# Optimization experiments

Hardware: AMD Instinct MI355X
Metric: run time of the kernel (lower is better)

The kernel has to match this reference:

```python
import jax, jax.numpy as jnp
import numpy as np

D_MODEL = 1024
NHEAD = 16
D_K = D_MODEL // NHEAD


def setup_inputs() -> dict:
    key = jax.random.key(0)
    ks = jax.random.split(key, 11)
    B, S = 2, 2048
    scale = 1.0 / np.sqrt(D_MODEL)
    inp = {
        "q": jax.random.normal(ks[0], (B, S, D_MODEL), jnp.float32),
        "k": jax.random.normal(ks[1], (B, S, D_MODEL), jnp.float32),
        "v": jax.random.normal(ks[2], (B, S, D_MODEL), jnp.float32),
        "Wq": jax.random.normal(ks[3], (D_MODEL, D_MODEL), jnp.float32) * scale,
        "bq": jnp.zeros((D_MODEL,), jnp.float32),
        "Wk": jax.random.normal(ks[4], (D_MODEL, D_MODEL), jnp.float32) * scale,
        "bk": jnp.zeros((D_MODEL,), jnp.float32),
        "Wv": jax.random.normal(ks[5], (D_MODEL, D_MODEL), jnp.float32) * scale,
        "bv": jnp.zeros((D_MODEL,), jnp.float32),
        "Wo": jax.random.normal(ks[6], (D_MODEL, D_MODEL), jnp.float32) * scale,
        "bo": jnp.zeros((D_MODEL,), jnp.float32),
    }
    return inp


def reference(q, k, v, Wq, bq, Wk, bk, Wv, bv, Wo, bo):
    B, S, _ = q.shape
    # Linear projections (torch Linear: x @ W.T + b), split into heads
    def proj(x, W, b):
        y = jnp.einsum('bsd,ed->bse', x, W) + b
        return y.reshape(B, -1, NHEAD, D_K).transpose(0, 2, 1, 3)  # [B,H,S,Dk]

    qh = proj(q, Wq, bq)
    kh = proj(k, Wk, bk)
    vh = proj(v, Wv, bv)

    scores = jnp.einsum('bhqd,bhkd->bhqk', qh, kh) / jnp.sqrt(
        jnp.asarray(D_K, qh.dtype))
    attn = jax.nn.softmax(scores, axis=-1)  # dropout is identity in eval
    out = jnp.einsum('bhqk,bhkd->bhqd', attn, vh)
    out = out.transpose(0, 2, 1, 3).reshape(B, S, D_MODEL)
    return jnp.einsum('bsd,ed->bse', out, Wo) + bo
```

## Files before the change

### kernel.cpp

```cpp
#include <hip/hip_runtime.h>
#include <stdint.h>
#include <stddef.h>

#define D_MODEL 1024
#define NHEAD   16
#define DK      64
#define BB      2
#define SS      2048
#define NTOK    (BB*SS)

#define SCALE_Q 0.18033688011f

typedef short  short8 __attribute__((ext_vector_type(8)));
typedef __bf16 bf16x8 __attribute__((ext_vector_type(8)));
typedef float  f32x4  __attribute__((ext_vector_type(4)));

__device__ __forceinline__ unsigned short f2bf(float x){
  unsigned int u = __builtin_bit_cast(unsigned int, x);
  u += 0x7fffu + ((u >> 16) & 1u);
  return (unsigned short)(u >> 16);
}

__device__ __forceinline__ unsigned int pack_bf2(float x, float y){
  unsigned int a = __builtin_bit_cast(unsigned int, x) + 0x8000u;
  unsigned int b = __builtin_bit_cast(unsigned int, y) + 0x8000u;
  return __builtin_amdgcn_perm(b, a, 0x07060302u);
}

__device__ __forceinline__ float fast_exp2(float x){
#if __has_builtin(__builtin_amdgcn_exp2f)
  return __builtin_amdgcn_exp2f(x);
#else
  return exp2f(x);
#endif
}

__device__ __forceinline__ f32x4 mfma16(bf16x8 a, bf16x8 b, f32x4 c){
  return __builtin_amdgcn_mfma_f32_16x16x32_bf16(a, b, c, 0, 0, 0);
}

__device__ __forceinline__ void async16(const void* g, void* lds){
  __builtin_amdgcn_global_load_lds(
      (const __attribute__((address_space(1))) unsigned int*)g,
      (__attribute__((address_space(3))) unsigned int*)lds,
      16, 0, 0);
}

__global__ __launch_bounds__(256) void cast_bf16_all(
    const float* __restrict__ q,  const float* __restrict__ k,  const float* __restrict__ v,
    const float* __restrict__ wq, const float* __restrict__ wk, const float* __restrict__ wv,
    const float* __restrict__ wo,
    unsigned short* __restrict__ qb,  unsigned short* __restrict__ kb,  unsigned short* __restrict__ vb,
    unsigned short* __restrict__ wqb, unsigned short* __restrict__ wkb, unsigned short* __restrict__ wvb,
    unsigned short* __restrict__ wob)
{
  const float* src; unsigned short* dst; int n;
  switch (blockIdx.y){
    case 0: src = q;  dst = qb;  n = NTOK*D_MODEL;    break;
    case 1: src = k;  dst = kb;  n = NTOK*D_MODEL;    break;
    case 2: src = v;  dst = vb;  n = NTOK*D_MODEL;    break;
    case 3: src = wq; dst = wqb; n = D_MODEL*D_MODEL; break;
    case 4: src = wk; dst = wkb; n = D_MODEL*D_MODEL; break;
    case 5: src = wv; dst = wvb; n = D_MODEL*D_MODEL; break;
    default: src = wo; dst = wob; n = D_MODEL*D_MODEL; break;
  }
  int i = (blockIdx.x * 256 + threadIdx.x) * 8;
  if (i >= n) return;
  float4 a = *(const float4*)(src + i);
  float4 b = *(const float4*)(src + i + 4);
  short8 o;
  o[0] = (short)f2bf(a.x); o[1] = (short)f2bf(a.y);
  o[2] = (short)f2bf(a.z); o[3] = (short)f2bf(a.w);
  o[4] = (short)f2bf(b.x); o[5] = (short)f2bf(b.y);
  o[6] = (short)f2bf(b.z); o[7] = (short)f2bf(b.w);
  *(short8*)(dst + i) = o;
}

__global__ __launch_bounds__(256) void qkv_gemm(
    const unsigned short* __restrict__ qb, const unsigned short* __restrict__ kb,
    const unsigned short* __restrict__ vb,
    const unsigned short* __restrict__ wqb, const unsigned short* __restrict__ wkb,
    const unsigned short* __restrict__ wvb,
    const float* __restrict__ bq, const float* __restrict__ bk, const float* __restrict__ bv,
    unsigned short* __restrict__ Qh, unsigned short* __restrict__ Kh, unsigned short* __restrict__ Vt)
{
  __shared__ __align__(16) unsigned short As[128*32];
  __shared__ __align__(16) unsigned short Bs[128*32];
  const int id = blockIdx.x, z = id >> 8, r = id & 255;
  const unsigned short *A, *Bt; const float* bias; unsigned short* C;
  int bm, bn, N, brow; float scale;
  if (z == 0){ A = qb;  Bt = wqb; bias = bq; C = Qh; bm = (r>>3)*128; bn = (r&7)*128; N = 1024; brow = 0; scale = SCALE_Q; }
  else if (z == 1){ A = kb;  Bt = wkb; bias = bk; C = Kh; bm = (r>>3)*128; bn = (r&7)*128; N = 1024; brow = 0; scale = 1.0f; }
  else            { A = wvb; Bt = vb;  bias = bv; C = Vt; bm = (r&7)*128; bn = (r>>3)*128; N = 4096; brow = 1; scale = 1.0f; }
  const int K = 1024;
  const int tid  = threadIdx.x, lane = tid & 63, w = tid >> 6;
  const int quad = lane >> 4,   l16  = lane & 15;
  const int wm = w >> 1, wn = w & 1;
  const int sw = l16 & 3;
  f32x4 acc[4][4] = {};
  for (int kb_ = 0; kb_ < (K >> 5); ++kb_){
    const int k0 = kb_ << 5;
    __syncthreads();
    #pragma unroll
    for (int c = 0; c < 2; ++c){
      int chunk = (w*2 + c)*64 + lane;
      int row = chunk >> 2, c4 = chunk & 3;
      int cs = (c4 ^ (row & 3)) << 3;
      async16(A  + (size_t)(bm + row)*K + k0 + cs, (char*)As + (w*2 + c)*1024);
      async16(Bt + (size_t)(bn + row)*K + k0 + cs, (char*)Bs + (w*2 + c)*1024);
    }
    __syncthreads();
    bf16x8 af[4], bf[4];
    #pragma unroll
    for (int mt = 0; mt < 4; ++mt)
      af[mt] = *(const bf16x8*)&As[(wm*64 + mt*16 + l16)*32 + ((quad ^ sw) << 3)];
    #pragma unroll
    for (int nt = 0; nt < 4; ++nt)
      bf[nt] = *(const bf16x8*)&Bs[(wn*64 + nt*16 + l16)*32 + ((quad ^ sw) << 3)];
    #pragma unroll
    for (int mt = 0; mt < 4; ++mt)
      #pragma unroll
      for (int nt = 0; nt < 4; ++nt)
        acc[mt][nt] = mfma16(af[mt], bf[nt], acc[mt][nt]);
  }
  const int m0 = bm + wm*64, n0 = bn + wn*64;
  #pragma unroll
  for (int mt = 0; mt < 4; ++mt){
    #pragma unroll
    for (int nt = 0; nt < 4; ++nt){
      int col = n0 + nt*16 + l16;
      float bc = brow ? 0.0f : bias[col];
      #pragma unroll
      for (int rr = 0; rr < 4; ++rr){
        int row = m0 + mt*16 + quad*4 + rr;
        float val = (acc[mt][nt][rr] + (brow ? bias[row] : bc)) * scale;
        C[(size_t)row*N + col] = f2bf(val);
      }
    }
  }
}

__global__ __launch_bounds__(256) void gemm_out(
    const unsigned short* __restrict__ A, const unsigned short* __restrict__ Bt,
    const float* __restrict__ bias, float* __restrict__ C)
{
  __shared__ __align__(16) unsigned short As[64*32];
  __shared__ __align__(16) unsigned short Bs[128*32];
  const int K = 1024, N = 1024;
  const int tid  = threadIdx.x, lane = tid & 63, w = tid >> 6;
  const int quad = lane >> 4,   l16  = lane & 15;
  const int bm = blockIdx.y * 64, bn = blockIdx.x * 128;
  const int sw = l16 & 3;
  f32x4 acc[4][2] = {};
  for (int kb_ = 0; kb_ < (K >> 5); ++kb_){
    const int k0 = kb_ << 5;
    __syncthreads();
    {
      int chunk = w*64 + lane;
      int row = chunk >> 2, c4 = chunk & 3;
      async16(A + (size_t)(bm + row)*K + k0 + ((c4 ^ (row & 3)) << 3),
              (char*)As + w*1024);
    }
    #pragma unroll
    for (int c = 0; c < 2; ++c){
      int chunk = (w*2 + c)*64 + lane;
      int row = chunk >> 2, c4 = chunk & 3;
      async16(Bt + (size_t)(bn + row)*K + k0 + ((c4 ^ (row & 3)) << 3),
              (char*)Bs + (w*2 + c)*1024);
    }
    __syncthreads();
    bf16x8 af[4], bf[2];
    #pragma unroll
    for (int mt = 0; mt < 4; ++mt)
      af[mt] = *(const bf16x8*)&As[(mt*16 + l16)*32 + ((quad ^ sw) << 3)];
    #pragma unroll
    for (int nt = 0; nt < 2; ++nt)
      bf[nt] = *(const bf16x8*)&Bs[(w*32 + nt*16 + l16)*32 + ((quad ^ sw) << 3)];
    #pragma unroll
    for (int mt = 0; mt < 4; ++mt)
      #pragma unroll
      for (int nt = 0; nt < 2; ++nt)
        acc[mt][nt] = mfma16(af[mt], bf[nt], acc[mt][nt]);
  }
  #pragma unroll
  for (int mt = 0; mt < 4; ++mt){
    #pragma unroll
    for (int nt = 0; nt < 2; ++nt){
      int col = bn + w*32 + nt*16 + l16;
      float bc = bias[col];
      #pragma unroll
      for (int rr = 0; rr < 4; ++rr){
        int row = bm + mt*16 + quad*4 + rr;
        C[(size_t)row*N + col] = acc[mt][nt][rr] + bc;
      }
    }
  }
}

__global__ __launch_bounds__(256) void attn(
    const unsigned short* __restrict__ Qh, const unsigned short* __restrict__ Kh,
    const unsigned short* __restrict__ Vt, unsigned short* __restrict__ ctx)
{
  __shared__ __align__(16) unsigned short Kbuf[64*64];
  __shared__ __align__(16) unsigned short Vbuf[64*64];
  __shared__ __align__(16) unsigned short QP[128*64];

  const int tid  = threadIdx.x, lane = tid & 63, w = tid >> 6;
  const int quad = lane >> 4,   l16  = lane & 15;
  const int b = blockIdx.y >> 4, h = blockIdx.y & 15;
  const int q0 = blockIdx.x * 128;
  const int sw = l16 & 7;

  #pragma unroll
  for (int c = 0; c < 4; ++c){
    int s = (w*4 + c)*64 + lane;
    int row = s >> 3, c8 = s & 7;
    async16(Qh + (size_t)(b*SS + q0 + row)*D_MODEL + h*DK + ((c8 ^ (row & 7)) << 3),
            (char*)QP + (w*4 + c)*1024);
  }
  __syncthreads();
  bf16x8 bq[2][2];
  #pragma unroll
  for (int qg = 0; qg < 2; ++qg)
    #pragma unroll
    for (int ks = 0; ks < 2; ++ks)
      bq[qg][ks] = *(const bf16x8*)&QP[(w*32 + qg*16 + l16)*64 + (((ks*4 + quad) ^ sw) << 3)];

  const unsigned short* Kp = Kh + (size_t)(b*SS)*D_MODEL + h*DK;
  const unsigned short* Vp = Vt + (size_t)(h*DK)*NTOK + b*SS;
  const unsigned short* ksrc[2];
  const unsigned short* vsrc[2];
  #pragma unroll
  for (int c = 0; c < 2; ++c){
    int s = (w*2 + c)*64 + lane;
    int row = s >> 3, c8 = s & 7;
    int cs = (c8 ^ (row & 7)) << 3;
    ksrc[c] = Kp + (size_t)row*D_MODEL + cs;
    vsrc[c] = Vp + (size_t)row*NTOK  + cs;
  }

  f32x4 acc[2][4] = {};
  float l_i[2] = {0.0f, 0.0f};

  for (int kv0 = 0; kv0 < SS; kv0 += 64){
    __syncthreads();
    #pragma unroll
    for (int c = 0; c < 2; ++c){
      async16(ksrc[c], (char*)Kbuf + (w*2 + c)*1024);
      async16(vsrc[c], (char*)Vbuf + (w*2 + c)*1024);
      ksrc[c] += 64*D_MODEL;
      vsrc[c] += 64;
    }
    __syncthreads();

    bf16x8 kf[4][2];
    #pragma unroll
    for (int mt = 0; mt < 4; ++mt)
      #pragma unroll
      for (int ks = 0; ks < 2; ++ks)
        kf[mt][ks] = *(const bf16x8*)&Kbuf[(mt*16 + l16)*64 + (((ks*4 + quad) ^ sw) << 3)];
    f32x4 s0[4] = {}, s1[4] = {};
    #pragma unroll
    for (int mt = 0; mt < 4; ++mt)
      #pragma unroll
      for (int ks = 0; ks < 2; ++ks){
        s0[mt] = mfma16(kf[mt][ks], bq[0][ks], s0[mt]);
        s1[mt] = mfma16(kf[mt][ks], bq[1][ks], s1[mt]);
      }

    float ls0 = 0.0f, ls1 = 0.0f;
    #pragma unroll
    for (int mt = 0; mt < 4; ++mt)
      #pragma unroll
      for (int rr = 0; rr < 4; ++rr){
        float p0 = fast_exp2(s0[mt][rr]); s0[mt][rr] = p0; ls0 += p0;
        float p1 = fast_exp2(s1[mt][rr]); s1[mt][rr] = p1; ls1 += p1;
      }
    l_i[0] += ls0; l_i[1] += ls1;
    const int pr0 = (w*32 +      l16)*64;
    const int pr1 = (w*32 + 16 + l16)*64;
    #pragma unroll
    for (int mt = 0; mt < 4; ++mt){
      int c8  = mt*2 + (quad >> 1);
      int off = ((c8 ^ sw) << 3) + (quad & 1)*4;
      uint2 p;
      p.x = pack_bf2(s0[mt][0], s0[mt][1]);
      p.y = pack_bf2(s0[mt][2], s0[mt][3]);
      *(uint2*)&QP[pr0 + off] = p;
      p.x = pack_bf2(s1[mt][0], s1[mt][1]);
      p.y = pack_bf2(s1[mt][2], s1[mt][3]);
      *(uint2*)&QP[pr1 + off] = p;
    }
    asm volatile("s_waitcnt lgkmcnt(0)" ::: "memory");

    bf16x8 bp[2][2];
    #pragma unroll
    for (int qg = 0; qg < 2; ++qg)
      #pragma unroll
      for (int ks = 0; ks < 2; ++ks)
        bp[qg][ks] = *(const bf16x8*)&QP[(w*32 + qg*16 + l16)*64 + (((ks*4 + quad) ^ sw) << 3)];
    bf16x8 vf[4][2];
    #pragma unroll
    for (int nt = 0; nt < 4; ++nt)
      #pragma unroll
      for (int ks = 0; ks < 2; ++ks)
        vf[nt][ks] = *(const bf16x8*)&Vbuf[(nt*16 + l16)*64 + (((ks*4 + quad) ^ sw) << 3)];
    #pragma unroll
    for (int nt = 0; nt < 4; ++nt)
      #pragma unroll
      for (int ks = 0; ks < 2; ++ks){
        acc[0][nt] = mfma16(vf[nt][ks], bp[0][ks], acc[0][nt]);
        acc[1][nt] = mfma16(vf[nt][ks], bp[1][ks], acc[1][nt]);
      }
  }

  float inv[2];
  #pragma unroll
  for (int qg = 0; qg < 2; ++qg){
    float t = l_i[qg];
    t += __shfl_xor(t, 16);
    t += __shfl_xor(t, 32);
    inv[qg] = 1.0f / t;
  }
  #pragma unroll
  for (int qg = 0; qg < 2; ++qg){
    int pr = (w*32 + qg*16 + l16)*64;
    #pragma unroll
    for (int nt = 0; nt < 4; ++nt){
      int c8  = nt*2 + (quad >> 1);
      int off = ((c8 ^ sw) << 3) + (quad & 1)*4;
      uint2 p;
      p.x = pack_bf2(acc[qg][nt][0]*inv[qg], acc[qg][nt][1]*inv[qg]);
      p.y = pack_bf2(acc[qg][nt][2]*inv[qg], acc[qg][nt][3]*inv[qg]);
      *(uint2*)&QP[pr + off] = p;
    }
  }
  asm volatile("s_waitcnt lgkmcnt(0)" ::: "memory");
  {
    int r  = w*32 + (lane >> 1);
    int j0 = (lane & 1)*4;
    unsigned short* dst = ctx + (size_t)(b*SS + q0 + r)*D_MODEL + h*DK;
    #pragma unroll
    for (int i = 0; i < 4; ++i){
      int j = j0 + i;
      uint4 d = *(const uint4*)&QP[r*64 + ((j ^ (r & 7)) << 3)];
      *(uint4*)(dst + j*8) = d;
    }
  }
}

extern "C" void kernel_launch(void* const* d_in, const int* in_sizes, int n_in,
                              void* d_out, int out_size, void* d_ws, size_t ws_size,
                              hipStream_t stream) {
  const float* q  = (const float*)d_in[0];
  const float* k  = (const float*)d_in[1];
  const float* v  = (const float*)d_in[2];
  const float* Wq = (const float*)d_in[3];
  const float* bq = (const float*)d_in[4];
  const float* Wk = (const float*)d_in[5];
  const float* bk = (const float*)d_in[6];
  const float* Wv = (const float*)d_in[7];
  const float* bv = (const float*)d_in[8];
  const float* Wo = (const float*)d_in[9];
  const float* bo = (const float*)d_in[10];

  char* ws = (char*)d_ws;
  const size_t TOKB = (size_t)NTOK * D_MODEL * 2;
  const size_t WB   = (size_t)D_MODEL * D_MODEL * 2;
  unsigned short* qb  = (unsigned short*)ws;             ws += TOKB;
  unsigned short* kb  = (unsigned short*)ws;             ws += TOKB;
  unsigned short* vb  = (unsigned short*)ws;             ws += TOKB;
  unsigned short* wqb = (unsigned short*)ws;             ws += WB;
  unsigned short* wkb = (unsigned short*)ws;             ws += WB;
  unsigned short* wvb = (unsigned short*)ws;             ws += WB;
  unsigned short* wob = (unsigned short*)ws;             ws += WB;
  unsigned short* Qh  = (unsigned short*)ws;             ws += TOKB;
  unsigned short* Kh  = (unsigned short*)ws;             ws += TOKB;
  unsigned short* Vt  = (unsigned short*)ws;             ws += TOKB;
  unsigned short* ctx = (unsigned short*)ws;             ws += TOKB;

  cast_bf16_all<<<dim3(2048, 7), 256, 0, stream>>>(q, k, v, Wq, Wk, Wv, Wo,
                                                   qb, kb, vb, wqb, wkb, wvb, wob);
  qkv_gemm<<<dim3(768), 256, 0, stream>>>(qb, kb, vb, wqb, wkb, wvb,
                                          bq, bk, bv, Qh, Kh, Vt);
  attn<<<dim3(SS/128, BB*NHEAD), 256, 0, stream>>>(Qh, Kh, Vt, ctx);
  gemm_out<<<dim3(8, 64), 256, 0, stream>>>(ctx, wob, bo, (float*)d_out);
}
```

Baseline: 237.6 us.

## Split attention KV range across two blocks with combine kernel; deepen GEMM K-tiles

The attention kernel now splits the 2048-key sequence into two halves via a third grid dimension. Each half writes unnormalized fp32 partial outputs and row sums to workspace, and a new combine kernel sums and normalizes them into the bf16 context. This doubles the attention grid from 512 to 1024 blocks for better CU occupancy, at the cost of extra fp32 global traffic and an added kernel launch. It appears to assume no running-max rescaling, so summing the two partials is enough. Separately, both GEMMs move from 32-wide to 64-wide K tiles with an 8-way swizzle, halving the number of barrier-separated iterations, and the workspace layout is reorganized so Op aliases the dead cast buffers.

```diff
diff --git a/kernel.cpp b/kernel.cpp
--- a/kernel.cpp
+++ b/kernel.cpp
@@ -84,8 +84,8 @@
     const float* __restrict__ bq, const float* __restrict__ bk, const float* __restrict__ bv,
     unsigned short* __restrict__ Qh, unsigned short* __restrict__ Kh, unsigned short* __restrict__ Vt)
 {
-  __shared__ __align__(16) unsigned short As[128*32];
-  __shared__ __align__(16) unsigned short Bs[128*32];
+  __shared__ __align__(16) unsigned short As[128*64];
+  __shared__ __align__(16) unsigned short Bs[128*64];
   const int id = blockIdx.x, z = id >> 8, r = id & 255;
   const unsigned short *A, *Bt; const float* bias; unsigned short* C;
   int bm, bn, N, brow; float scale;
@@ -96,32 +96,36 @@
   const int tid  = threadIdx.x, lane = tid & 63, w = tid >> 6;
   const int quad = lane >> 4,   l16  = lane & 15;
   const int wm = w >> 1, wn = w & 1;
-  const int sw = l16 & 3;
+  const int sw = l16 & 7;
   f32x4 acc[4][4] = {};
-  for (int kb_ = 0; kb_ < (K >> 5); ++kb_){
-    const int k0 = kb_ << 5;
-    __syncthreads();
-    #pragma unroll
-    for (int c = 0; c < 2; ++c){
-      int chunk = (w*2 + c)*64 + lane;
-      int row = chunk >> 2, c4 = chunk & 3;
-      int cs = (c4 ^ (row & 3)) << 3;
-      async16(A  + (size_t)(bm + row)*K + k0 + cs, (char*)As + (w*2 + c)*1024);
-      async16(Bt + (size_t)(bn + row)*K + k0 + cs, (char*)Bs + (w*2 + c)*1024);
-    }
-    __syncthreads();
-    bf16x8 af[4], bf[4];
+  for (int kb_ = 0; kb_ < 16; ++kb_){
+    const int k0 = kb_ << 6;
+    __syncthreads();
+    #pragma unroll
+    for (int c = 0; c < 4; ++c){
+      int chunk = (w*4 + c)*64 + lane;
+      int row = chunk >> 3, c8 = chunk & 7;
+      int cs = (c8 ^ (row & 7)) << 3;
+      async16(A  + (size_t)(bm + row)*K + k0 + cs, (char*)As + (w*4 + c)*1024);
+      async16(Bt + (size_t)(bn + row)*K + k0 + cs, (char*)Bs + (w*4 + c)*1024);
+    }
+    __syncthreads();
+    bf16x8 af[4][2], bf[4][2];
     #pragma unroll
     for (int mt = 0; mt < 4; ++mt)
-      af[mt] = *(const bf16x8*)&As[(wm*64 + mt*16 + l16)*32 + ((quad ^ sw) << 3)];
-    #pragma unroll
-    for (int nt = 0; nt < 4; ++nt)
-      bf[nt] = *(const bf16x8*)&Bs[(wn*64 + nt*16 + l16)*32 + ((quad ^ sw) << 3)];
-    #pragma unroll
-    for (int mt = 0; mt < 4; ++mt)
-      #pragma unroll
-      for (int nt = 0; nt < 4; ++nt)
-        acc[mt][nt] = mfma16(af[mt], bf[nt], acc[mt][nt]);
+      #pragma unroll
+      for (int ks = 0; ks < 2; ++ks){
+        int off = (((ks*4 + quad) ^ sw) << 3);
+        af[mt][ks] = *(const bf16x8*)&As[(wm*64 + mt*16 + l16)*64 + off];
+        bf[mt][ks] = *(const bf16x8*)&Bs[(wn*64 + mt*16 + l16)*64 + off];
+      }
+    #pragma unroll
+    for (int ks = 0; ks < 2; ++ks)
+      #pragma unroll
+      for (int mt = 0; mt < 4; ++mt)
+        #pragma unroll
+        for (int nt = 0; nt < 4; ++nt)
+          acc[mt][nt] = mfma16(af[mt][ks], bf[nt][ks], acc[mt][nt]);
   }
   const int m0 = bm + wm*64, n0 = bn + wn*64;
   #pragma unroll
@@ -144,43 +148,50 @@
     const unsigned short* __restrict__ A, const unsigned short* __restrict__ Bt,
     const float* __restrict__ bias, float* __restrict__ C)
 {
-  __shared__ __align__(16) unsigned short As[64*32];
-  __shared__ __align__(16) unsigned short Bs[128*32];
+  __shared__ __align__(16) unsigned short As[64*64];
+  __shared__ __align__(16) unsigned short Bs[128*64];
   const int K = 1024, N = 1024;
   const int tid  = threadIdx.x, lane = tid & 63, w = tid >> 6;
   const int quad = lane >> 4,   l16  = lane & 15;
   const int bm = blockIdx.y * 64, bn = blockIdx.x * 128;
-  const int sw = l16 & 3;
+  const int sw = l16 & 7;
   f32x4 acc[4][2] = {};
-  for (int kb_ = 0; kb_ < (K >> 5); ++kb_){
-    const int k0 = kb_ << 5;
-    __syncthreads();
-    {
-      int chunk = w*64 + lane;
-      int row = chunk >> 2, c4 = chunk & 3;
-      async16(A + (size_t)(bm + row)*K + k0 + ((c4 ^ (row & 3)) << 3),
-              (char*)As + w*1024);
-    }
+  for (int kb_ = 0; kb_ < 16; ++kb_){
+    const int k0 = kb_ << 6;
+    __syncthreads();
     #pragma unroll
     for (int c = 0; c < 2; ++c){
       int chunk = (w*2 + c)*64 + lane;
-      int row = chunk >> 2, c4 = chunk & 3;
-      async16(Bt + (size_t)(bn + row)*K + k0 + ((c4 ^ (row & 3)) << 3),
-              (char*)Bs + (w*2 + c)*1024);
-    }
-    __syncthreads();
-    bf16x8 af[4], bf[2];
+      int row = chunk >> 3, c8 = chunk & 7;
+      async16(A + (size_t)(bm + row)*K + k0 + ((c8 ^ (row & 7)) << 3),
+              (char*)As + (w*2 + c)*1024);
+    }
+    #pragma unroll
+    for (int c = 0; c < 4; ++c){
+      int chunk = (w*4 + c)*64 + lane;
+      int row = chunk >> 3, c8 = chunk & 7;
+      async16(Bt + (size_t)(bn + row)*K + k0 + ((c8 ^ (row & 7)) << 3),
+              (char*)Bs + (w*4 + c)*1024);
+    }
+    __syncthreads();
+    bf16x8 af[4][2], bf[2][2];
     #pragma unroll
     for (int mt = 0; mt < 4; ++mt)
-      af[mt] = *(const bf16x8*)&As[(mt*16 + l16)*32 + ((quad ^ sw) << 3)];
+      #pragma unroll
+      for (int ks = 0; ks < 2; ++ks)
+        af[mt][ks] = *(const bf16x8*)&As[(mt*16 + l16)*64 + (((ks*4 + quad) ^ sw) << 3)];
     #pragma unroll
     for (int nt = 0; nt < 2; ++nt)
-      bf[nt] = *(const bf16x8*)&Bs[(w*32 + nt*16 + l16)*32 + ((quad ^ sw) << 3)];
-    #pragma unroll
-    for (int mt = 0; mt < 4; ++mt)
-      #pragma unroll
-      for (int nt = 0; nt < 2; ++nt)
-        acc[mt][nt] = mfma16(af[mt], bf[nt], acc[mt][nt]);
+      #pragma unroll
+      for (int ks = 0; ks < 2; ++ks)
+        bf[nt][ks] = *(const bf16x8*)&Bs[(w*32 + nt*16 + l16)*64 + (((ks*4 + quad) ^ sw) << 3)];
+    #pragma unroll
+    for (int ks = 0; ks < 2; ++ks)
+      #pragma unroll
+      for (int mt = 0; mt < 4; ++mt)
+        #pragma unroll
+        for (int nt = 0; nt < 2; ++nt)
+          acc[mt][nt] = mfma16(af[mt][ks], bf[nt][ks], acc[mt][nt]);
   }
   #pragma unroll
   for (int mt = 0; mt < 4; ++mt){
@@ -199,16 +210,19 @@
 
 __global__ __launch_bounds__(256) void attn(
     const unsigned short* __restrict__ Qh, const unsigned short* __restrict__ Kh,
-    const unsigned short* __restrict__ Vt, unsigned short* __restrict__ ctx)
+    const unsigned short* __restrict__ Vt,
+    float* __restrict__ Op, float* __restrict__ lp)
 {
-  __shared__ __align__(16) unsigned short Kbuf[64*64];
-  __shared__ __align__(16) unsigned short Vbuf[64*64];
-  __shared__ __align__(16) unsigned short QP[128*64];
+  __shared__ __align__(16) char smem[32768];
+  unsigned short* Kbuf = (unsigned short*)smem;
+  unsigned short* Vbuf = (unsigned short*)(smem + 8192);
+  unsigned short* QP   = (unsigned short*)(smem + 16384);
 
   const int tid  = threadIdx.x, lane = tid & 63, w = tid >> 6;
   const int quad = lane >> 4,   l16  = lane & 15;
-  const int b = blockIdx.y >> 4, h = blockIdx.y & 15;
+  const int bh = blockIdx.y, b = bh >> 4, h = bh & 15;
   const int q0 = blockIdx.x * 128;
+  const int part = blockIdx.z;
   const int sw = l16 & 7;
 
   #pragma unroll
@@ -235,14 +249,14 @@
     int s = (w*2 + c)*64 + lane;
     int row = s >> 3, c8 = s & 7;
     int cs = (c8 ^ (row & 7)) << 3;
-    ksrc[c] = Kp + (size_t)row*D_MODEL + cs;
-    vsrc[c] = Vp + (size_t)row*NTOK  + cs;
+    ksrc[c] = Kp + (size_t)(part*1024 + row)*D_MODEL + cs;
+    vsrc[c] = Vp + (size_t)row*NTOK + part*1024 + cs;
   }
 
   f32x4 acc[2][4] = {};
   float l_i[2] = {0.0f, 0.0f};
 
-  for (int kv0 = 0; kv0 < SS; kv0 += 64){
+  for (int it = 0; it < 16; ++it){
     __syncthreads();
     #pragma unroll
     for (int c = 0; c < 2; ++c){
@@ -314,39 +328,61 @@
       }
   }
 
-  float inv[2];
+  float lred[2];
   #pragma unroll
   for (int qg = 0; qg < 2; ++qg){
     float t = l_i[qg];
     t += __shfl_xor(t, 16);
     t += __shfl_xor(t, 32);
-    inv[qg] = 1.0f / t;
-  }
-  #pragma unroll
-  for (int qg = 0; qg < 2; ++qg){
-    int pr = (w*32 + qg*16 + l16)*64;
-    #pragma unroll
-    for (int nt = 0; nt < 4; ++nt){
-      int c8  = nt*2 + (quad >> 1);
-      int off = ((c8 ^ sw) << 3) + (quad & 1)*4;
-      uint2 p;
-      p.x = pack_bf2(acc[qg][nt][0]*inv[qg], acc[qg][nt][1]*inv[qg]);
-      p.y = pack_bf2(acc[qg][nt][2]*inv[qg], acc[qg][nt][3]*inv[qg]);
-      *(uint2*)&QP[pr + off] = p;
-    }
-  }
-  asm volatile("s_waitcnt lgkmcnt(0)" ::: "memory");
-  {
-    int r  = w*32 + (lane >> 1);
-    int j0 = (lane & 1)*4;
-    unsigned short* dst = ctx + (size_t)(b*SS + q0 + r)*D_MODEL + h*DK;
-    #pragma unroll
-    for (int i = 0; i < 4; ++i){
-      int j = j0 + i;
-      uint4 d = *(const uint4*)&QP[r*64 + ((j ^ (r & 7)) << 3)];
-      *(uint4*)(dst + j*8) = d;
-    }
-  }
+    lred[qg] = t;
+  }
+  if (quad == 0){
+    #pragma unroll
+    for (int qg = 0; qg < 2; ++qg)
+      lp[(size_t)part*(32*SS) + (size_t)bh*SS + q0 + w*32 + qg*16 + l16] = lred[qg];
+  }
+
+  float* F = (float*)smem;
+  float* myOp = Op + (size_t)part*((size_t)32*SS*DK) + ((size_t)bh*SS + q0)*DK;
+  #pragma unroll
+  for (int ph = 0; ph < 2; ++ph){
+    __syncthreads();
+    if ((w >> 1) == ph){
+      #pragma unroll
+      for (int qg = 0; qg < 2; ++qg){
+        int fr = (w & 1)*32 + qg*16 + l16;
+        #pragma unroll
+        for (int nt = 0; nt < 4; ++nt)
+          *(f32x4*)&F[fr*68 + nt*16 + quad*4] = acc[qg][nt];
+      }
+    }
+    __syncthreads();
+    int row = tid >> 2, cb = (tid & 3)*16;
+    float* dst = myOp + (size_t)(ph*64 + row)*DK;
+    #pragma unroll
+    for (int i = 0; i < 4; ++i)
+      *(f32x4*)(dst + cb + i*4) = *(const f32x4*)&F[row*68 + cb + i*4];
+  }
+}
+
+__global__ __launch_bounds__(256) void combine(
+    const float* __restrict__ Op, const float* __restrict__ lp,
+    unsigned short* __restrict__ ctx)
+{
+  const size_t OPS = (size_t)32*SS*DK;
+  int t = blockIdx.x;
+  int b = t >> 11, s = t & (SS-1);
+  int f = threadIdx.x * 4;
+  int h = f >> 6, dk = f & 63;
+  size_t o = ((size_t)(b*16 + h)*SS + s)*DK + dk;
+  f32x4 o0 = *(const f32x4*)&Op[o];
+  f32x4 o1 = *(const f32x4*)&Op[OPS + o];
+  size_t li = (size_t)(b*16 + h)*SS + s;
+  float inv = 1.0f / (lp[li] + lp[(size_t)32*SS + li]);
+  uint2 r;
+  r.x = pack_bf2((o0[0]+o1[0])*inv, (o0[1]+o1[1])*inv);
+  r.y = pack_bf2((o0[2]+o1[2])*inv, (o0[3]+o1[3])*inv);
+  *(uint2*)&ctx[(size_t)t*D_MODEL + f] = r;
 }
 
 extern "C" void kernel_launch(void* const* d_in, const int* in_sizes, int n_in,
@@ -364,25 +400,28 @@
   const float* Wo = (const float*)d_in[9];
   const float* bo = (const float*)d_in[10];
 
+  const size_t MB = 1024*1024;
   char* ws = (char*)d_ws;
-  const size_t TOKB = (size_t)NTOK * D_MODEL * 2;
-  const size_t WB   = (size_t)D_MODEL * D_MODEL * 2;
-  unsigned short* qb  = (unsigned short*)ws;             ws += TOKB;
-  unsigned short* kb  = (unsigned short*)ws;             ws += TOKB;
-  unsigned short* vb  = (unsigned short*)ws;             ws += TOKB;
-  unsigned short* wqb = (unsigned short*)ws;             ws += WB;
-  unsigned short* wkb = (unsigned short*)ws;             ws += WB;
-  unsigned short* wvb = (unsigned short*)ws;             ws += WB;
-  unsigned short* wob = (unsigned short*)ws;             ws += WB;
-  unsigned short* Qh  = (unsigned short*)ws;             ws += TOKB;
-  unsigned short* Kh  = (unsigned short*)ws;             ws += TOKB;
-  unsigned short* Vt  = (unsigned short*)ws;             ws += TOKB;
-  unsigned short* ctx = (unsigned short*)ws;             ws += TOKB;
+  unsigned short* wob = (unsigned short*)(ws);
+  unsigned short* Qh  = (unsigned short*)(ws + 2*MB);
+  unsigned short* Kh  = (unsigned short*)(ws + 10*MB);
+  unsigned short* Vt  = (unsigned short*)(ws + 18*MB);
+  unsigned short* ctx = (unsigned short*)(ws + 26*MB);
+  float*          lp  = (float*)(ws + 34*MB);
+  char* S = ws + 35*MB;
+  unsigned short* qb  = (unsigned short*)(S);
+  unsigned short* kb  = (unsigned short*)(S + 8*MB);
+  unsigned short* vb  = (unsigned short*)(S + 16*MB);
+  unsigned short* wqb = (unsigned short*)(S + 24*MB);
+  unsigned short* wkb = (unsigned short*)(S + 26*MB);
+  unsigned short* wvb = (unsigned short*)(S + 28*MB);
+  float*          Op  = (float*)(S);
 
   cast_bf16_all<<<dim3(2048, 7), 256, 0, stream>>>(q, k, v, Wq, Wk, Wv, Wo,
                                                    qb, kb, vb, wqb, wkb, wvb, wob);
   qkv_gemm<<<dim3(768), 256, 0, stream>>>(qb, kb, vb, wqb, wkb, wvb,
                                           bq, bk, bv, Qh, Kh, Vt);
-  attn<<<dim3(SS/128, BB*NHEAD), 256, 0, stream>>>(Qh, Kh, Vt, ctx);
+  attn<<<dim3(SS/128, BB*NHEAD, 2), 256, 0, stream>>>(Qh, Kh, Vt, Op, lp);
+  combine<<<dim3(NTOK), 256, 0, stream>>>(Op, lp, ctx);
   gemm_out<<<dim3(8, 64), 256, 0, stream>>>(ctx, wob, bo, (float*)d_out);
 }
```

Result: slower. 243.4 us (+2.4%).

## Widen GEMM K-tile to 64 and restructure attention loop per query group

Applied to the files above, without the earlier changes.

Both projection GEMMs now stage 64-wide K slices in shared memory instead of 32, using an 8-way XOR swizzle. This halves the number of barrier pairs and gives each loaded tile twice as many MFMAs. Separately, the attention inner loop processes the two query groups one after another (score, exp, pack, then PV), replacing the explicit lgkmcnt wait with a compiler memory barrier. This should lower live register pressure and let work from one group overlap with the other. The cost is doubled LDS per GEMM block, which may reduce occupancy.

```diff
diff --git a/kernel.cpp b/kernel.cpp
--- a/kernel.cpp
+++ b/kernel.cpp
@@ -84,8 +84,8 @@
     const float* __restrict__ bq, const float* __restrict__ bk, const float* __restrict__ bv,
     unsigned short* __restrict__ Qh, unsigned short* __restrict__ Kh, unsigned short* __restrict__ Vt)
 {
-  __shared__ __align__(16) unsigned short As[128*32];
-  __shared__ __align__(16) unsigned short Bs[128*32];
+  __shared__ __align__(16) unsigned short As[128*64];
+  __shared__ __align__(16) unsigned short Bs[128*64];
   const int id = blockIdx.x, z = id >> 8, r = id & 255;
   const unsigned short *A, *Bt; const float* bias; unsigned short* C;
   int bm, bn, N, brow; float scale;
@@ -96,32 +96,36 @@
   const int tid  = threadIdx.x, lane = tid & 63, w = tid >> 6;
   const int quad = lane >> 4,   l16  = lane & 15;
   const int wm = w >> 1, wn = w & 1;
-  const int sw = l16 & 3;
+  const int sw = l16 & 7;
   f32x4 acc[4][4] = {};
-  for (int kb_ = 0; kb_ < (K >> 5); ++kb_){
-    const int k0 = kb_ << 5;
-    __syncthreads();
-    #pragma unroll
-    for (int c = 0; c < 2; ++c){
-      int chunk = (w*2 + c)*64 + lane;
-      int row = chunk >> 2, c4 = chunk & 3;
-      int cs = (c4 ^ (row & 3)) << 3;
-      async16(A  + (size_t)(bm + row)*K + k0 + cs, (char*)As + (w*2 + c)*1024);
-      async16(Bt + (size_t)(bn + row)*K + k0 + cs, (char*)Bs + (w*2 + c)*1024);
-    }
-    __syncthreads();
-    bf16x8 af[4], bf[4];
+  for (int kb_ = 0; kb_ < 16; ++kb_){
+    const int k0 = kb_ << 6;
+    __syncthreads();
+    #pragma unroll
+    for (int c = 0; c < 4; ++c){
+      int chunk = (w*4 + c)*64 + lane;
+      int row = chunk >> 3, c8 = chunk & 7;
+      int cs = (c8 ^ (row & 7)) << 3;
+      async16(A  + (size_t)(bm + row)*K + k0 + cs, (char*)As + (w*4 + c)*1024);
+      async16(Bt + (size_t)(bn + row)*K + k0 + cs, (char*)Bs + (w*4 + c)*1024);
+    }
+    __syncthreads();
+    bf16x8 af[4][2], bf[4][2];
     #pragma unroll
     for (int mt = 0; mt < 4; ++mt)
-      af[mt] = *(const bf16x8*)&As[(wm*64 + mt*16 + l16)*32 + ((quad ^ sw) << 3)];
-    #pragma unroll
-    for (int nt = 0; nt < 4; ++nt)
-      bf[nt] = *(const bf16x8*)&Bs[(wn*64 + nt*16 + l16)*32 + ((quad ^ sw) << 3)];
-    #pragma unroll
-    for (int mt = 0; mt < 4; ++mt)
-      #pragma unroll
-      for (int nt = 0; nt < 4; ++nt)
-        acc[mt][nt] = mfma16(af[mt], bf[nt], acc[mt][nt]);
+      #pragma unroll
+      for (int ks = 0; ks < 2; ++ks){
+        int off = (((ks*4 + quad) ^ sw) << 3);
+        af[mt][ks] = *(const bf16x8*)&As[(wm*64 + mt*16 + l16)*64 + off];
+        bf[mt][ks] = *(const bf16x8*)&Bs[(wn*64 + mt*16 + l16)*64 + off];
+      }
+    #pragma unroll
+    for (int ks = 0; ks < 2; ++ks)
+      #pragma unroll
+      for (int mt = 0; mt < 4; ++mt)
+        #pragma unroll
+        for (int nt = 0; nt < 4; ++nt)
+          acc[mt][nt] = mfma16(af[mt][ks], bf[nt][ks], acc[mt][nt]);
   }
   const int m0 = bm + wm*64, n0 = bn + wn*64;
   #pragma unroll
@@ -144,43 +148,50 @@
     const unsigned short* __restrict__ A, const unsigned short* __restrict__ Bt,
     const float* __restrict__ bias, float* __restrict__ C)
 {
-  __shared__ __align__(16) unsigned short As[64*32];
-  __shared__ __align__(16) unsigned short Bs[128*32];
+  __shared__ __align__(16) unsigned short As[64*64];
+  __shared__ __align__(16) unsigned short Bs[128*64];
   const int K = 1024, N = 1024;
   const int tid  = threadIdx.x, lane = tid & 63, w = tid >> 6;
   const int quad = lane >> 4,   l16  = lane & 15;
   const int bm = blockIdx.y * 64, bn = blockIdx.x * 128;
-  const int sw = l16 & 3;
+  const int sw = l16 & 7;
   f32x4 acc[4][2] = {};
-  for (int kb_ = 0; kb_ < (K >> 5); ++kb_){
-    const int k0 = kb_ << 5;
-    __syncthreads();
-    {
-      int chunk = w*64 + lane;
-      int row = chunk >> 2, c4 = chunk & 3;
-      async16(A + (size_t)(bm + row)*K + k0 + ((c4 ^ (row & 3)) << 3),
-              (char*)As + w*1024);
-    }
+  for (int kb_ = 0; kb_ < 16; ++kb_){
+    const int k0 = kb_ << 6;
+    __syncthreads();
     #pragma unroll
     for (int c = 0; c < 2; ++c){
       int chunk = (w*2 + c)*64 + lane;
-      int row = chunk >> 2, c4 = chunk & 3;
-      async16(Bt + (size_t)(bn + row)*K + k0 + ((c4 ^ (row & 3)) << 3),
-              (char*)Bs + (w*2 + c)*1024);
-    }
-    __syncthreads();
-    bf16x8 af[4], bf[2];
+      int row = chunk >> 3, c8 = chunk & 7;
+      async16(A + (size_t)(bm + row)*K + k0 + ((c8 ^ (row & 7)) << 3),
+              (char*)As + (w*2 + c)*1024);
+    }
+    #pragma unroll
+    for (int c = 0; c < 4; ++c){
+      int chunk = (w*4 + c)*64 + lane;
+      int row = chunk >> 3, c8 = chunk & 7;
+      async16(Bt + (size_t)(bn + row)*K + k0 + ((c8 ^ (row & 7)) << 3),
+              (char*)Bs + (w*4 + c)*1024);
+    }
+    __syncthreads();
+    bf16x8 af[4][2], bf[2][2];
     #pragma unroll
     for (int mt = 0; mt < 4; ++mt)
-      af[mt] = *(const bf16x8*)&As[(mt*16 + l16)*32 + ((quad ^ sw) << 3)];
+      #pragma unroll
+      for (int ks = 0; ks < 2; ++ks)
+        af[mt][ks] = *(const bf16x8*)&As[(mt*16 + l16)*64 + (((ks*4 + quad) ^ sw) << 3)];
     #pragma unroll
     for (int nt = 0; nt < 2; ++nt)
-      bf[nt] = *(const bf16x8*)&Bs[(w*32 + nt*16 + l16)*32 + ((quad ^ sw) << 3)];
-    #pragma unroll
-    for (int mt = 0; mt < 4; ++mt)
-      #pragma unroll
-      for (int nt = 0; nt < 2; ++nt)
-        acc[mt][nt] = mfma16(af[mt], bf[nt], acc[mt][nt]);
+      #pragma unroll
+      for (int ks = 0; ks < 2; ++ks)
+        bf[nt][ks] = *(const bf16x8*)&Bs[(w*32 + nt*16 + l16)*64 + (((ks*4 + quad) ^ sw) << 3)];
+    #pragma unroll
+    for (int ks = 0; ks < 2; ++ks)
+      #pragma unroll
+      for (int mt = 0; mt < 4; ++mt)
+        #pragma unroll
+        for (int nt = 0; nt < 2; ++nt)
+          acc[mt][nt] = mfma16(af[mt][ks], bf[nt][ks], acc[mt][nt]);
   }
   #pragma unroll
   for (int mt = 0; mt < 4; ++mt){
@@ -259,46 +270,36 @@
       #pragma unroll
       for (int ks = 0; ks < 2; ++ks)
         kf[mt][ks] = *(const bf16x8*)&Kbuf[(mt*16 + l16)*64 + (((ks*4 + quad) ^ sw) << 3)];
-    f32x4 s0[4] = {}, s1[4] = {};
-    #pragma unroll
-    for (int mt = 0; mt < 4; ++mt)
-      #pragma unroll
-      for (int ks = 0; ks < 2; ++ks){
-        s0[mt] = mfma16(kf[mt][ks], bq[0][ks], s0[mt]);
-        s1[mt] = mfma16(kf[mt][ks], bq[1][ks], s1[mt]);
+
+    #pragma unroll
+    for (int qg = 0; qg < 2; ++qg){
+      f32x4 s[4] = {};
+      #pragma unroll
+      for (int mt = 0; mt < 4; ++mt)
+        #pragma unroll
+        for (int ks = 0; ks < 2; ++ks)
+          s[mt] = mfma16(kf[mt][ks], bq[qg][ks], s[mt]);
+      float ls = 0.0f;
+      #pragma unroll
+      for (int mt = 0; mt < 4; ++mt)
+        #pragma unroll
+        for (int rr = 0; rr < 4; ++rr){
+          float p = fast_exp2(s[mt][rr]); s[mt][rr] = p; ls += p;
+        }
+      l_i[qg] += ls;
+      const int pr = (w*32 + qg*16 + l16)*64;
+      #pragma unroll
+      for (int mt = 0; mt < 4; ++mt){
+        int c8  = mt*2 + (quad >> 1);
+        int off = ((c8 ^ sw) << 3) + (quad & 1)*4;
+        uint2 p;
+        p.x = pack_bf2(s[mt][0], s[mt][1]);
+        p.y = pack_bf2(s[mt][2], s[mt][3]);
+        *(uint2*)&QP[pr + off] = p;
       }
-
-    float ls0 = 0.0f, ls1 = 0.0f;
-    #pragma unroll
-    for (int mt = 0; mt < 4; ++mt)
-      #pragma unroll
-      for (int rr = 0; rr < 4; ++rr){
-        float p0 = fast_exp2(s0[mt][rr]); s0[mt][rr] = p0; ls0 += p0;
-        float p1 = fast_exp2(s1[mt][rr]); s1[mt][rr] = p1; ls1 += p1;
-      }
-    l_i[0] += ls0; l_i[1] += ls1;
-    const int pr0 = (w*32 +      l16)*64;
-    const int pr1 = (w*32 + 16 + l16)*64;
-    #pragma unroll
-    for (int mt = 0; mt < 4; ++mt){
-      int c8  = mt*2 + (quad >> 1);
-      int off = ((c8 ^ sw) << 3) + (quad & 1)*4;
-      uint2 p;
-      p.x = pack_bf2(s0[mt][0], s0[mt][1]);
-      p.y = pack_bf2(s0[mt][2], s0[mt][3]);
-      *(uint2*)&QP[pr0 + off] = p;
-      p.x = pack_bf2(s1[mt][0], s1[mt][1]);
-      p.y = pack_bf2(s1[mt][2], s1[mt][3]);
-      *(uint2*)&QP[pr1 + off] = p;
-    }
-    asm volatile("s_waitcnt lgkmcnt(0)" ::: "memory");
-
-    bf16x8 bp[2][2];
-    #pragma unroll
-    for (int qg = 0; qg < 2; ++qg)
-      #pragma unroll
-      for (int ks = 0; ks < 2; ++ks)
-        bp[qg][ks] = *(const bf16x8*)&QP[(w*32 + qg*16 + l16)*64 + (((ks*4 + quad) ^ sw) << 3)];
+    }
+    asm volatile("" ::: "memory");
+
     bf16x8 vf[4][2];
     #pragma unroll
     for (int nt = 0; nt < 4; ++nt)
@@ -306,12 +307,17 @@
       for (int ks = 0; ks < 2; ++ks)
         vf[nt][ks] = *(const bf16x8*)&Vbuf[(nt*16 + l16)*64 + (((ks*4 + quad) ^ sw) << 3)];
     #pragma unroll
-    for (int nt = 0; nt < 4; ++nt)
-      #pragma unroll
-      for (int ks = 0; ks < 2; ++ks){
-        acc[0][nt] = mfma16(vf[nt][ks], bp[0][ks], acc[0][nt]);
-        acc[1][nt] = mfma16(vf[nt][ks], bp[1][ks], acc[1][nt]);
-      }
+    for (int qg = 0; qg < 2; ++qg){
+      bf16x8 bp[2];
+      #pragma unroll
+      for (int ks = 0; ks < 2; ++ks)
+        bp[ks] = *(const bf16x8*)&QP[(w*32 + qg*16 + l16)*64 + (((ks*4 + quad) ^ sw) << 3)];
+      #pragma unroll
+      for (int nt = 0; nt < 4; ++nt)
+        #pragma unroll
+        for (int ks = 0; ks < 2; ++ks)
+          acc[qg][nt] = mfma16(vf[nt][ks], bp[ks], acc[qg][nt]);
+    }
   }
 
   float inv[2];
```

New measurement: 235.2 us. No clear change (-1.0%).
